# Kernel optimization log

Measured on AMD Instinct MI355X. Metric: run time of the kernel, lower is better.

Reference implementation:

```python
import jax, jax.numpy as jnp
import numpy as np

N, D, H, R = 50000, 256, 4, 3
C = D // H        # head dim = 64
E = 400000        # edges per relation
NEG = 0.2         # LeakyReLU slope
LN_EPS = 1e-5


def _segment_softmax(att, seg, n):
    # att: [E, H], seg: [E] destination node ids -> softmax per (node, head)
    m = jax.ops.segment_max(att, seg, num_segments=n)
    m = jnp.where(jnp.isfinite(m), m, 0.0)        # nodes with no edges
    e = jnp.exp(att - m[seg])
    s = jax.ops.segment_sum(e, seg, num_segments=n)
    return e / (s[seg] + 1e-16)


def setup_inputs() -> dict:
    key = jax.random.key(0)
    ks = jax.random.split(key, 16)
    inp = {
        'feat': jax.random.normal(ks[0], (N, D), jnp.float32),
        'Wl': jax.random.normal(ks[1], (D, D), jnp.float32) / np.sqrt(D).astype(np.float32),
        'bl': jnp.zeros((D,), jnp.float32),
        'Wr': jax.random.normal(ks[2], (D, D), jnp.float32) / np.sqrt(D).astype(np.float32),
        'br': jnp.zeros((D,), jnp.float32),
        'attn_l': jax.random.normal(ks[3], (R, H, C), jnp.float32) / np.sqrt(C).astype(np.float32),
        'attn_r': jax.random.normal(ks[4], (R, H, C), jnp.float32) / np.sqrt(C).astype(np.float32),
        'rel_q': jax.random.normal(ks[5], (H, C), jnp.float32) / np.sqrt(C).astype(np.float32),
        'rel_k': jax.random.normal(ks[6], (H, C), jnp.float32) / np.sqrt(C).astype(np.float32),
        'ln_gamma': jnp.ones((D,), jnp.float32),
        'ln_beta': jnp.zeros((D,), jnp.float32),
    }
    for r in range(R):
        inp[f'edge_src_{r}'] = jax.random.randint(ks[7 + 2 * r], (E,), 0, N, jnp.int64 if jax.config.jax_enable_x64 else jnp.int32)
        inp[f'edge_dst_{r}'] = jax.random.randint(ks[8 + 2 * r], (E,), 0, N, jnp.int64 if jax.config.jax_enable_x64 else jnp.int32)
    return inp


def reference(feat, Wl, bl, Wr, br, attn_l, attn_r, rel_q, rel_k, ln_gamma, ln_beta,
              edge_src_0, edge_dst_0, edge_src_1, edge_dst_1, edge_src_2, edge_dst_2):
    # per-node-type linear projections -> multi-head [N, H, C]
    k = (feat @ Wl + bl).reshape(N, H, C)
    v = (feat @ Wr + br).reshape(N, H, C)
    srcs = [edge_src_0, edge_src_1, edge_src_2]
    dsts = [edge_dst_0, edge_dst_1, edge_dst_2]
    rel_outs = []
    for r in range(R):  # loop over fixed, structurally distinct relations
        s, d = srcs[r], dsts[r]
        # edge attention: (k_src . a_l) + (v_dst . a_r), LeakyReLU (attn_dropout inactive in eval)
        att = jnp.einsum('ehc,hc->eh', k[s], attn_l[r]) + jnp.einsum('ehc,hc->eh', v[d], attn_r[r])
        att = jax.nn.leaky_relu(att, NEG)
        a = _segment_softmax(att, d, N)                                   # [E, H]
        # message 'h' is edges.dst['v'] in the original code (faithful)
        h = jax.ops.segment_sum(a[:, :, None] * v[d], d, num_segments=N)  # [N, H, C]
        rel_outs.append(h)
    # stack relation embeddings + self 'v' (the +1 none-selection relation)
    x = jnp.stack(rel_outs + [v], axis=1)                                  # [N, T=R+1, H, C]
    # MetapathGATConv (1 layer) stand-in: self embedding queries all relations per head
    q = jnp.einsum('nhc,hc->nh', x[:, -1], rel_q)                          # [N, H]
    kk = jnp.einsum('nthc,hc->nth', x, rel_k)                              # [N, T, H]
    beta = jax.nn.softmax(jax.nn.leaky_relu(q[:, None, :] + kk, NEG), axis=1)  # [N, T, H]
    out = jnp.einsum('nth,nthc->nhc', beta, x).reshape(N, D)
    # activation -> (dropout inactive in eval) -> LayerNorm
    out = jax.nn.relu(out)
    mu = out.mean(-1, keepdims=True)
    var = out.var(-1, keepdims=True)
    out = (out - mu) * jax.lax.rsqrt(var + LN_EPS) * ln_gamma + ln_beta
    return out
```

## Files before the change

### kernel.cpp

```cpp
#include <hip/hip_runtime.h>

#define N_NODES 50000
#define DIM 256
#define NEG 0.2f
#define LN_EPS 1e-5f
#define SCAT_BLOCKS 2048

typedef __attribute__((ext_vector_type(8))) short short8;
typedef __attribute__((ext_vector_type(4))) float f32x4;

__device__ __forceinline__ unsigned short f2bf(float x) {
    unsigned int u = __builtin_bit_cast(unsigned int, x);
    u += 0x7fffu + ((u >> 16) & 1u);
    return (unsigned short)(u >> 16);
}

__device__ __forceinline__ void load_lds16(const void* g, void* l) {
    __builtin_amdgcn_global_load_lds((const unsigned int*)g, (unsigned int*)l, 16, 0, 0);
}

__device__ __forceinline__ short8 cvt_bfrag(float4 a4, float4 b4) {
    short8 r;
    r[0] = (short)f2bf(a4.x); r[1] = (short)f2bf(a4.y);
    r[2] = (short)f2bf(a4.z); r[3] = (short)f2bf(a4.w);
    r[4] = (short)f2bf(b4.x); r[5] = (short)f2bf(b4.y);
    r[6] = (short)f2bf(b4.z); r[7] = (short)f2bf(b4.w);
    return r;
}

__global__ __launch_bounds__(256) void prep(
    const float* __restrict__ Wr, unsigned short* __restrict__ WrF,
    const int* __restrict__ d0, const int* __restrict__ d1, const int* __restrict__ d2,
    int E, unsigned char* __restrict__ mask)
{
    if (blockIdx.x < 32) {
        const int o    = blockIdx.x * 256 + threadIdx.x;
        const int lane = o & 63;
        const int frag = o >> 6;
        const int mt = frag & 15, kk = frag >> 4;
        const int ln = lane & 15, quad = lane >> 4;
        const float* src = Wr + (size_t)(kk * 32 + quad * 8) * DIM + mt * 16 + ln;
        short8 v;
        #pragma unroll
        for (int j = 0; j < 8; ++j) v[j] = (short)f2bf(src[(size_t)j * DIM]);
        *(short8*)(WrF + (size_t)o * 8) = v;
    } else {
        const int total = 3 * E;
        for (int i = (blockIdx.x - 32) * 256 + (int)threadIdx.x; i < total;
             i += SCAT_BLOCKS * 256) {
            const int* d; int base, e;
            if (i >= 2 * E)  { d = d2; e = i - 2 * E; base = 2 * N_NODES; }
            else if (i >= E) { d = d1; e = i - E;     base = N_NODES; }
            else             { d = d0; e = i;         base = 0; }
            mask[base + d[e]] = (unsigned char)1;
        }
    }
}

__global__ __launch_bounds__(256, 4) void fused_mfma(
    const float* __restrict__ feat, const unsigned short* __restrict__ WrF,
    const float* __restrict__ br, const float* __restrict__ rel_q,
    const float* __restrict__ rel_k, const float* __restrict__ gamma,
    const float* __restrict__ beta_p, const unsigned char* __restrict__ mask,
    float* __restrict__ out)
{
    __shared__ unsigned short lds[2][8192];
    const int lane = threadIdx.x & 63;
    const int wave = threadIdx.x >> 6;
    const int ln = lane & 15;
    const int quad = lane >> 4;
    int node = blockIdx.x * 64 + wave * 16 + ln;
    const bool valid = node < N_NODES;
    if (!valid) node = N_NODES - 1;

    const float* fptr = feat + (size_t)node * DIM + quad * 8;

    float4 FA[2], FB[2];
    FA[0] = *(const float4*)(fptr);       FB[0] = *(const float4*)(fptr + 4);
    FA[1] = *(const float4*)(fptr + 32);  FB[1] = *(const float4*)(fptr + 36);

    {
        const char* g = (const char*)WrF;
        #pragma unroll
        for (int r = 0; r < 4; ++r) {
            const int off = wave * 4096 + r * 1024;
            load_lds16(g + off + lane * 16, (char*)lds[0] + off);
        }
    }

    const int m0 = (int)mask[node];
    const int m1 = (int)mask[N_NODES + node];
    const int m2 = (int)mask[2 * N_NODES + node];

    f32x4 acc[16];
    #pragma unroll
    for (int mt = 0; mt < 16; ++mt) acc[mt] = (f32x4){0.f, 0.f, 0.f, 0.f};

    short8 bcur = cvt_bfrag(FA[0], FB[0]);

    __syncthreads();

    #pragma unroll
    for (int p = 0; p < 8; ++p) {
        if (p < 7) {
            const char* g = (const char*)WrF + (p + 1) * 16384;
            char* l = (char*)lds[(p + 1) & 1];
            #pragma unroll
            for (int r = 0; r < 4; ++r) {
                const int off = wave * 4096 + r * 1024;
                load_lds16(g + off + lane * 16, l + off);
            }
        }
        if (p < 6) {
            FA[p & 1] = *(const float4*)(fptr + (p + 2) * 32);
            FB[p & 1] = *(const float4*)(fptr + (p + 2) * 32 + 4);
        }
        const char* b = (const char*)lds[p & 1];
        #pragma unroll
        for (int mt = 0; mt < 16; ++mt) {
            const short8 a = *(const short8*)(b + mt * 1024 + lane * 16);
            acc[mt] = __builtin_amdgcn_mfma_f32_16x16x32_bf16(a, bcur, acc[mt], 0, 0, 0);
        }
        if (p < 7) {
            bcur = cvt_bfrag(FA[(p + 1) & 1], FB[(p + 1) & 1]);
            __syncthreads();
        }
    }

    float qp[4] = {0.f, 0.f, 0.f, 0.f}, kp[4] = {0.f, 0.f, 0.f, 0.f};
    #pragma unroll
    for (int mt = 0; mt < 16; ++mt) {
        const int cbase = mt * 16 + quad * 4;
        const float4 bb = *(const float4*)(br + cbase);
        acc[mt][0] += bb.x; acc[mt][1] += bb.y; acc[mt][2] += bb.z; acc[mt][3] += bb.w;
        const float4 rq = *(const float4*)(rel_q + cbase);
        const float4 rk = *(const float4*)(rel_k + cbase);
        const int h = mt >> 2;
        qp[h] += acc[mt][0] * rq.x + acc[mt][1] * rq.y + acc[mt][2] * rq.z + acc[mt][3] * rq.w;
        kp[h] += acc[mt][0] * rk.x + acc[mt][1] * rk.y + acc[mt][2] * rk.z + acc[mt][3] * rk.w;
    }
    #pragma unroll
    for (int h = 0; h < 4; ++h) {
        qp[h] += __shfl_xor(qp[h], 16); qp[h] += __shfl_xor(qp[h], 32);
        kp[h] += __shfl_xor(kp[h], 16); kp[h] += __shfl_xor(kp[h], 32);
    }

    const int cnt = m0 + m1 + m2;

    float wgt[4];
    #pragma unroll
    for (int h = 0; h < 4; ++h) {
        const float q = qp[h];
        const float qk = q + kp[h];
        const float a = q  > 0.f ? q  : NEG * q;
        const float b = qk > 0.f ? qk : NEG * qk;
        const float mx = fmaxf(a, b);
        const float eb = (float)(cnt + 1) * __expf(b - mx);
        const float ea = (float)(3 - cnt) * __expf(a - mx);
        wgt[h] = eb / (eb + ea);
    }

    float sum = 0.f, ssq = 0.f;
    #pragma unroll
    for (int mt = 0; mt < 16; ++mt) {
        const float w = wgt[mt >> 2];
        #pragma unroll
        for (int r = 0; r < 4; ++r) {
            float v = fmaxf(acc[mt][r] * w, 0.f);
            acc[mt][r] = v;
            sum += v; ssq += v * v;
        }
    }
    sum += __shfl_xor(sum, 16); sum += __shfl_xor(sum, 32);
    ssq += __shfl_xor(ssq, 16); ssq += __shfl_xor(ssq, 32);
    const float mu = sum * (1.f / 256.f);
    const float var = ssq * (1.f / 256.f) - mu * mu;
    const float rstd = rsqrtf(var + LN_EPS);

    if (valid) {
        float* optr = out + (size_t)node * DIM;
        #pragma unroll
        for (int mt = 0; mt < 16; ++mt) {
            const int cbase = mt * 16 + quad * 4;
            const float4 g = *(const float4*)(gamma + cbase);
            const float4 b = *(const float4*)(beta_p + cbase);
            float4 r;
            r.x = (acc[mt][0] - mu) * rstd * g.x + b.x;
            r.y = (acc[mt][1] - mu) * rstd * g.y + b.y;
            r.z = (acc[mt][2] - mu) * rstd * g.z + b.z;
            r.w = (acc[mt][3] - mu) * rstd * g.w + b.w;
            *(float4*)(optr + cbase) = r;
        }
    }
}

extern "C" void kernel_launch(void* const* d_in, const int* in_sizes, int n_in,
                              void* d_out, int out_size, void* d_ws, size_t ws_size,
                              hipStream_t stream) {
    const float* feat  = (const float*)d_in[0];
    const float* Wr    = (const float*)d_in[3];
    const float* br    = (const float*)d_in[4];
    const float* rel_q = (const float*)d_in[7];
    const float* rel_k = (const float*)d_in[8];
    const float* gamma = (const float*)d_in[9];
    const float* beta  = (const float*)d_in[10];
    const int* dst0 = (const int*)d_in[12];
    const int* dst1 = (const int*)d_in[14];
    const int* dst2 = (const int*)d_in[16];
    const int E = in_sizes[12];

    unsigned short* WrF = (unsigned short*)d_ws;
    unsigned char* mask = (unsigned char*)d_ws + DIM * DIM * 2;

    hipMemsetAsync(mask, 0, 150016, stream);
    prep<<<32 + SCAT_BLOCKS, 256, 0, stream>>>(Wr, WrF, dst0, dst1, dst2, E, mask);
    fused_mfma<<<(N_NODES + 63) / 64, 256, 0, stream>>>(
        feat, WrF, br, rel_q, rel_k, gamma, beta, mask, (float*)d_out);
}
```

Measured before the change: 176.8 us.

## Split output columns across wave pairs, halving nodes per block

Each block now handles 32 nodes instead of 64. Two waves share each 16-node group, and each wave computes half of the 256 output columns, so it holds 8 accumulator tiles instead of 16. All eight bf16 feature fragments are loaded and converted up front rather than streamed inside the loop. The LayerNorm sum and sum of squares are combined across the wave pair through LDS with an extra barrier. This cuts register pressure and doubles the block count, at the cost of loading the full weight matrix into LDS twice as many times overall.

```diff
diff --git a/kernel.cpp b/kernel.cpp
--- a/kernel.cpp
+++ b/kernel.cpp
@@ -64,27 +64,23 @@
     const float* __restrict__ beta_p, const unsigned char* __restrict__ mask,
     float* __restrict__ out)
 {
-    __shared__ unsigned short lds[2][8192];
+    __shared__ char lds[33280];
     const int lane = threadIdx.x & 63;
     const int wave = threadIdx.x >> 6;
+    const int mhalf = wave & 1;
+    const int ng = wave >> 1;
     const int ln = lane & 15;
     const int quad = lane >> 4;
-    int node = blockIdx.x * 64 + wave * 16 + ln;
+    int node = blockIdx.x * 32 + ng * 16 + ln;
     const bool valid = node < N_NODES;
     if (!valid) node = N_NODES - 1;
 
-    const float* fptr = feat + (size_t)node * DIM + quad * 8;
-
-    float4 FA[2], FB[2];
-    FA[0] = *(const float4*)(fptr);       FB[0] = *(const float4*)(fptr + 4);
-    FA[1] = *(const float4*)(fptr + 32);  FB[1] = *(const float4*)(fptr + 36);
-
     {
         const char* g = (const char*)WrF;
         #pragma unroll
         for (int r = 0; r < 4; ++r) {
             const int off = wave * 4096 + r * 1024;
-            load_lds16(g + off + lane * 16, (char*)lds[0] + off);
+            load_lds16(g + off + lane * 16, lds + off);
         }
     }
 
@@ -92,87 +88,103 @@
     const int m1 = (int)mask[N_NODES + node];
     const int m2 = (int)mask[2 * N_NODES + node];
 
-    f32x4 acc[16];
-    #pragma unroll
-    for (int mt = 0; mt < 16; ++mt) acc[mt] = (f32x4){0.f, 0.f, 0.f, 0.f};
-
-    short8 bcur = cvt_bfrag(FA[0], FB[0]);
+    const float* fptr = feat + (size_t)node * DIM + quad * 8;
+    short8 bfr[8];
+    #pragma unroll
+    for (int c = 0; c < 4; ++c) {
+        float4 F0[2], F1[2];
+        #pragma unroll
+        for (int k = 0; k < 2; ++k) {
+            F0[k] = *(const float4*)(fptr + (c * 2 + k) * 32);
+            F1[k] = *(const float4*)(fptr + (c * 2 + k) * 32 + 4);
+        }
+        #pragma unroll
+        for (int k = 0; k < 2; ++k) bfr[c * 2 + k] = cvt_bfrag(F0[k], F1[k]);
+    }
+
+    f32x4 acc[8];
+    #pragma unroll
+    for (int j = 0; j < 8; ++j) acc[j] = (f32x4){0.f, 0.f, 0.f, 0.f};
 
     __syncthreads();
 
     #pragma unroll
-    for (int p = 0; p < 8; ++p) {
-        if (p < 7) {
-            const char* g = (const char*)WrF + (p + 1) * 16384;
-            char* l = (char*)lds[(p + 1) & 1];
+    for (int kk = 0; kk < 8; ++kk) {
+        if (kk < 7) {
+            const char* g = (const char*)WrF + (kk + 1) * 16384;
+            char* l = lds + (((kk + 1) & 1) << 14);
             #pragma unroll
             for (int r = 0; r < 4; ++r) {
                 const int off = wave * 4096 + r * 1024;
                 load_lds16(g + off + lane * 16, l + off);
             }
         }
-        if (p < 6) {
-            FA[p & 1] = *(const float4*)(fptr + (p + 2) * 32);
-            FB[p & 1] = *(const float4*)(fptr + (p + 2) * 32 + 4);
-        }
-        const char* b = (const char*)lds[p & 1];
-        #pragma unroll
-        for (int mt = 0; mt < 16; ++mt) {
-            const short8 a = *(const short8*)(b + mt * 1024 + lane * 16);
-            acc[mt] = __builtin_amdgcn_mfma_f32_16x16x32_bf16(a, bcur, acc[mt], 0, 0, 0);
-        }
-        if (p < 7) {
-            bcur = cvt_bfrag(FA[(p + 1) & 1], FB[(p + 1) & 1]);
-            __syncthreads();
-        }
-    }
-
-    float qp[4] = {0.f, 0.f, 0.f, 0.f}, kp[4] = {0.f, 0.f, 0.f, 0.f};
-    #pragma unroll
-    for (int mt = 0; mt < 16; ++mt) {
-        const int cbase = mt * 16 + quad * 4;
+        const char* wb = lds + ((kk & 1) << 14) + mhalf * 8192 + lane * 16;
+        #pragma unroll
+        for (int j = 0; j < 8; ++j) {
+            const short8 a = *(const short8*)(wb + j * 1024);
+            acc[j] = __builtin_amdgcn_mfma_f32_16x16x32_bf16(a, bfr[kk], acc[j], 0, 0, 0);
+        }
+        if (kk < 7) __syncthreads();
+    }
+
+    float qp[2] = {0.f, 0.f}, kp[2] = {0.f, 0.f};
+    #pragma unroll
+    for (int j = 0; j < 8; ++j) {
+        const int cbase = (mhalf * 8 + j) * 16 + quad * 4;
         const float4 bb = *(const float4*)(br + cbase);
-        acc[mt][0] += bb.x; acc[mt][1] += bb.y; acc[mt][2] += bb.z; acc[mt][3] += bb.w;
+        acc[j][0] += bb.x; acc[j][1] += bb.y; acc[j][2] += bb.z; acc[j][3] += bb.w;
         const float4 rq = *(const float4*)(rel_q + cbase);
         const float4 rk = *(const float4*)(rel_k + cbase);
-        const int h = mt >> 2;
-        qp[h] += acc[mt][0] * rq.x + acc[mt][1] * rq.y + acc[mt][2] * rq.z + acc[mt][3] * rq.w;
-        kp[h] += acc[mt][0] * rk.x + acc[mt][1] * rk.y + acc[mt][2] * rk.z + acc[mt][3] * rk.w;
-    }
-    #pragma unroll
-    for (int h = 0; h < 4; ++h) {
-        qp[h] += __shfl_xor(qp[h], 16); qp[h] += __shfl_xor(qp[h], 32);
-        kp[h] += __shfl_xor(kp[h], 16); kp[h] += __shfl_xor(kp[h], 32);
+        const int hh = j >> 2;
+        qp[hh] += acc[j][0] * rq.x + acc[j][1] * rq.y + acc[j][2] * rq.z + acc[j][3] * rq.w;
+        kp[hh] += acc[j][0] * rk.x + acc[j][1] * rk.y + acc[j][2] * rk.z + acc[j][3] * rk.w;
+    }
+    #pragma unroll
+    for (int hh = 0; hh < 2; ++hh) {
+        qp[hh] += __shfl_xor(qp[hh], 16); qp[hh] += __shfl_xor(qp[hh], 32);
+        kp[hh] += __shfl_xor(kp[hh], 16); kp[hh] += __shfl_xor(kp[hh], 32);
     }
 
     const int cnt = m0 + m1 + m2;
 
-    float wgt[4];
-    #pragma unroll
-    for (int h = 0; h < 4; ++h) {
-        const float q = qp[h];
-        const float qk = q + kp[h];
+    float wgt[2];
+    #pragma unroll
+    for (int hh = 0; hh < 2; ++hh) {
+        const float q = qp[hh];
+        const float qk = q + kp[hh];
         const float a = q  > 0.f ? q  : NEG * q;
         const float b = qk > 0.f ? qk : NEG * qk;
         const float mx = fmaxf(a, b);
         const float eb = (float)(cnt + 1) * __expf(b - mx);
         const float ea = (float)(3 - cnt) * __expf(a - mx);
-        wgt[h] = eb / (eb + ea);
+        wgt[hh] = eb / (eb + ea);
     }
 
     float sum = 0.f, ssq = 0.f;
     #pragma unroll
-    for (int mt = 0; mt < 16; ++mt) {
-        const float w = wgt[mt >> 2];
+    for (int j = 0; j < 8; ++j) {
+        const float w = wgt[j >> 2];
         #pragma unroll
         for (int r = 0; r < 4; ++r) {
-            float v = fmaxf(acc[mt][r] * w, 0.f);
-            acc[mt][r] = v;
+            float v = fmaxf(acc[j][r] * w, 0.f);
+            acc[j][r] = v;
             sum += v; ssq += v * v;
         }
     }
     sum += __shfl_xor(sum, 16); sum += __shfl_xor(sum, 32);
     ssq += __shfl_xor(ssq, 16); ssq += __shfl_xor(ssq, 32);
+
+    float* ss = (float*)(lds + 32768);
+    if (quad == 0) {
+        const int idx = ((ng * 2 + mhalf) * 16 + ln) * 2;
+        ss[idx] = sum; ss[idx + 1] = ssq;
+    }
+    __syncthreads();
+    {
+        const int pidx = ((ng * 2 + (1 - mhalf)) * 16 + ln) * 2;
+        sum += ss[pidx]; ssq += ss[pidx + 1];
+    }
     const float mu = sum * (1.f / 256.f);
     const float var = ssq * (1.f / 256.f) - mu * mu;
     const float rstd = rsqrtf(var + LN_EPS);
@@ -180,15 +192,15 @@
     if (valid) {
         float* optr = out + (size_t)node * DIM;
         #pragma unroll
-        for (int mt = 0; mt < 16; ++mt) {
-            const int cbase = mt * 16 + quad * 4;
+        for (int j = 0; j < 8; ++j) {
+            const int cbase = (mhalf * 8 + j) * 16 + quad * 4;
             const float4 g = *(const float4*)(gamma + cbase);
             const float4 b = *(const float4*)(beta_p + cbase);
             float4 r;
-            r.x = (acc[mt][0] - mu) * rstd * g.x + b.x;
-            r.y = (acc[mt][1] - mu) * rstd * g.y + b.y;
-            r.z = (acc[mt][2] - mu) * rstd * g.z + b.z;
-            r.w = (acc[mt][3] - mu) * rstd * g.w + b.w;
+            r.x = (acc[j][0] - mu) * rstd * g.x + b.x;
+            r.y = (acc[j][1] - mu) * rstd * g.y + b.y;
+            r.z = (acc[j][2] - mu) * rstd * g.z + b.z;
+            r.w = (acc[j][3] - mu) * rstd * g.w + b.w;
             *(float4*)(optr + cbase) = r;
         }
     }
@@ -214,6 +226,6 @@
 
     hipMemsetAsync(mask, 0, 150016, stream);
     prep<<<32 + SCAT_BLOCKS, 256, 0, stream>>>(Wr, WrF, dst0, dst1, dst2, E, mask);
-    fused_mfma<<<(N_NODES + 63) / 64, 256, 0, stream>>>(
+    fused_mfma<<<(N_NODES + 31) / 32, 256, 0, stream>>>(
         feat, WrF, br, rel_q, rel_k, gamma, beta, mask, (float*)d_out);
 }
```

Result: faster. 163.5 us (-7.5%).
